# Kernel optimization log

Measured on AMD Instinct MI355X. Metric: run time of the kernel, lower is better.

## Reference

```python
import jax, jax.numpy as jnp
import numpy as np

THETA = 10000.0

def precompute_freqs_cis(dim, seq_len):
    freqs = 1.0 / THETA ** (jnp.arange(0, dim, 2)[: dim // 2].astype(jnp.float32) / dim)
    t = jnp.arange(seq_len, dtype=jnp.float32)
    ang = jnp.outer(t, freqs)  # [T, dim/2]
    return jax.lax.complex(jnp.cos(ang), jnp.sin(ang))

def apply_rope(x, freqs_cis):
    # x: [..., T, D]; freqs_cis: [T, D/2] complex
    xr = x.astype(jnp.float32).reshape(*x.shape[:-1], -1, 2)
    xc = jax.lax.complex(xr[..., 0], xr[..., 1]) * freqs_cis
    out = jnp.stack([jnp.real(xc), jnp.imag(xc)], axis=-1).reshape(x.shape)
    return out.astype(x.dtype)

def setup_inputs() -> dict:
    key = jax.random.key(0)
    k1, k2, k3, k4 = jax.random.split(key, 4)
    B, T, E, DQ, DV = 4, 2048, 1024, 128, 128
    s = 1.0 / np.sqrt(E)
    return {
        "embedding_word": jax.random.normal(k1, (B, T, E), dtype=jnp.float32),
        "w_Q": jax.random.normal(k2, (DQ, E), dtype=jnp.float32) * s,  # torch Linear weight [out,in]
        "w_K": jax.random.normal(k3, (DQ, E), dtype=jnp.float32) * s,
        "w_V": jax.random.normal(k4, (DV, E), dtype=jnp.float32) * s,
    }

def reference(embedding_word, w_Q, w_K, w_V):
    T = embedding_word.shape[-2]
    dq = w_Q.shape[0]
    q = jnp.einsum("bte,de->btd", embedding_word, w_Q)
    k = jnp.einsum("bte,de->btd", embedding_word, w_K)
    v = jnp.einsum("bte,de->btd", embedding_word, w_V)
    fc = precompute_freqs_cis(dq, T)
    q = apply_rope(q, fc)
    k = apply_rope(k, fc)
    scores = jnp.einsum("bqd,bkd->bqk", q, k)
    causal = jnp.triu(jnp.ones((T, T), dtype=bool), k=1)
    masked = jnp.where(causal, -jnp.inf, scores)
    weights = jax.nn.softmax(masked / jnp.sqrt(jnp.float32(dq)), axis=-1)
    return jnp.einsum("bqk,bkd->bqd", weights, v)
```

## Files before the change

### kernel.cpp

```cpp
#include <hip/hip_runtime.h>
#include <math.h>


#define B_ 4
#define T_ 2048
#define E_ 1024
#define D_ 128
#define BT_ (B_ * T_)

#define UNITS_PER_B 160
#define UNITS (UNITS_PER_B * B_)

typedef __bf16 bf16_t;
typedef __bf16 bf16x4 __attribute__((ext_vector_type(4)));
typedef __bf16 bf16x8 __attribute__((ext_vector_type(8)));
typedef float f32x4 __attribute__((ext_vector_type(4)));

#define GLD16(g, l)                                                         \
  __builtin_amdgcn_global_load_lds(                                         \
      (const __attribute__((address_space(1))) void*)(g),                   \
      (__attribute__((address_space(3))) void*)(l), 16, 0, 0)

__device__ __forceinline__ bf16x8 cvt8(float4 lo, float4 hi) {
  bf16x8 t;
  t[0] = (bf16_t)lo.x; t[1] = (bf16_t)lo.y; t[2] = (bf16_t)lo.z; t[3] = (bf16_t)lo.w;
  t[4] = (bf16_t)hi.x; t[5] = (bf16_t)hi.y; t[6] = (bf16_t)hi.z; t[7] = (bf16_t)hi.w;
  return t;
}
__device__ __forceinline__ bf16x8 cvt8v(f32x4 lo, f32x4 hi) {
  bf16x8 t;
  t[0] = (bf16_t)lo[0]; t[1] = (bf16_t)lo[1]; t[2] = (bf16_t)lo[2]; t[3] = (bf16_t)lo[3];
  t[4] = (bf16_t)hi[0]; t[5] = (bf16_t)hi[1]; t[6] = (bf16_t)hi[2]; t[7] = (bf16_t)hi[3];
  return t;
}

__global__ __launch_bounds__(256) void wtab_kernel(
    const float* __restrict__ Wq, const float* __restrict__ Wk,
    const float* __restrict__ Wv, bf16_t* __restrict__ Wb,
    float2* __restrict__ Tab) {
  const int gidx = blockIdx.x * 256 + threadIdx.x;
  if (gidx < 3 * D_ * E_ / 8) {
    const int z = gidx / 16384;
    const int r = gidx % 16384;
    const float* src = ((z == 0) ? Wq : (z == 1) ? Wk : Wv) + (size_t)r * 8;
    float4 u = *(const float4*)src;
    float4 v = *(const float4*)(src + 4);
    *(bf16x8*)(Wb + (size_t)z * D_ * E_ + (size_t)r * 8) = cvt8(u, v);
  }
  const float NLOG_ = -0.14391156514261485f;
  for (int idx = gidx; idx < T_ * 64; idx += 65536) {
    const int t = idx >> 6, j = idx & 63;
    const float freq = expf(NLOG_ * (float)j);
    float sn, cs;
    sincosf((float)t * freq, &sn, &cs);
    Tab[idx] = make_float2(cs, sn);
  }
}

__global__ __launch_bounds__(256) void proj64_kernel(
    const float* __restrict__ X, const bf16_t* __restrict__ Wb,
    const float2* __restrict__ Tab, bf16_t* __restrict__ Qws,
    bf16_t* __restrict__ Kws, bf16_t* __restrict__ Vtws) {
  const int o = blockIdx.x;
  const int ell = (o & 7) * 96 + (o >> 3);
  const int mt = ell / 6, ny = ell % 6;
  const int bt0 = mt * 64;

  const int tid = threadIdx.x;
  const int lane = tid & 63;
  const int wv = tid >> 6;
  const int wr = wv >> 1, wc = wv & 1;
  const int g = lane >> 4, lm = lane & 15;

  __shared__ float Axf[2][64 * 64];
  __shared__ bf16_t Bb[2][64 * 64];

  const bf16_t* Wz = Wb + (size_t)ny * 64 * E_;

  f32x4 acc[2][2];
#pragma unroll
  for (int m = 0; m < 2; m++)
#pragma unroll
    for (int n = 0; n < 2; n++) acc[m][n] = 0.0f;

  auto stage = [&](int t, int bf) {
    const int k0 = t * 64;
#pragma unroll
    for (int j = 0; j < 4; j++) {
      const int cb = (wv * 4 + j) * 64;
      const int L = cb + lane;
      const int row = L >> 4;
      const int pch = L & 15;
      const int c = pch ^ (row & 15);
      GLD16(X + (size_t)(bt0 + row) * E_ + k0 + c * 4, &Axf[bf][cb * 4]);
    }
#pragma unroll
    for (int j = 0; j < 2; j++) {
      const int cb = (wv * 2 + j) * 64;
      const int c = cb + lane;
      const int row = c >> 3;
      const int eoff = ((c & 7) * 8) ^ ((row & 7) << 3);
      GLD16(Wz + (size_t)row * E_ + k0 + eoff, &Bb[bf][cb * 8]);
    }
  };

  auto compute = [&](int bf) {
#pragma unroll
    for (int ks = 0; ks < 2; ks++) {
      const int cc = ks * 8 + g * 2;
      bf16x8 a0, a1, b0, b1;
      {
        const int r0 = wr * 32 + lm;
        f32x4 lo0 = *(const f32x4*)&Axf[bf][r0 * 64 + (cc ^ (r0 & 15)) * 4];
        f32x4 hi0 = *(const f32x4*)&Axf[bf][r0 * 64 + ((cc + 1) ^ (r0 & 15)) * 4];
        a0 = cvt8v(lo0, hi0);
        const int r1 = wr * 32 + 16 + lm;
        f32x4 lo1 = *(const f32x4*)&Axf[bf][r1 * 64 + (cc ^ (r1 & 15)) * 4];
        f32x4 hi1 = *(const f32x4*)&Axf[bf][r1 * 64 + ((cc + 1) ^ (r1 & 15)) * 4];
        a1 = cvt8v(lo1, hi1);
        const int s0 = wc * 32 + lm;
        b0 = *(const bf16x8*)&Bb[bf][s0 * 64 + ((ks * 32 + g * 8) ^ ((s0 & 7) << 3))];
        const int s1 = wc * 32 + 16 + lm;
        b1 = *(const bf16x8*)&Bb[bf][s1 * 64 + ((ks * 32 + g * 8) ^ ((s1 & 7) << 3))];
      }
      acc[0][0] = __builtin_amdgcn_mfma_f32_16x16x32_bf16(a0, b0, acc[0][0], 0, 0, 0);
      acc[0][1] = __builtin_amdgcn_mfma_f32_16x16x32_bf16(a0, b1, acc[0][1], 0, 0, 0);
      acc[1][0] = __builtin_amdgcn_mfma_f32_16x16x32_bf16(a1, b0, acc[1][0], 0, 0, 0);
      acc[1][1] = __builtin_amdgcn_mfma_f32_16x16x32_bf16(a1, b1, acc[1][1], 0, 0, 0);
    }
  };

  stage(0, 0);
  stage(1, 1);
  asm volatile("s_waitcnt vmcnt(6)" ::: "memory");
  __builtin_amdgcn_s_barrier();
  __builtin_amdgcn_sched_barrier(0);

#pragma unroll
  for (int t = 0; t < 16; t++) {
    compute(t & 1);
    __builtin_amdgcn_sched_barrier(0);
    __builtin_amdgcn_s_barrier();
    __builtin_amdgcn_sched_barrier(0);
    if (t + 2 < 16) {
      stage(t + 2, t & 1);
      asm volatile("s_waitcnt vmcnt(6)" ::: "memory");
    } else {
      asm volatile("s_waitcnt vmcnt(0)" ::: "memory");
    }
    __builtin_amdgcn_sched_barrier(0);
    __builtin_amdgcn_s_barrier();
    __builtin_amdgcn_sched_barrier(0);
  }

  const int b = bt0 >> 11;
#pragma unroll
  for (int nf = 0; nf < 2; nf++) {
    const int col = ny * 64 + wc * 32 + nf * 16 + lm;
    const int z = col >> 7;
    const int d = col & 127;
#pragma unroll
    for (int mf = 0; mf < 2; mf++) {
      const int row0 = bt0 + wr * 32 + mf * 16 + g * 4;
      if (z < 2) {
        bf16_t* dst = (z == 0) ? Qws : Kws;
#pragma unroll
        for (int r = 0; r < 4; r++) {
          const int bt = row0 + r;
          const int tt = bt & (T_ - 1);
          float val = acc[mf][nf][r];
          float prt = __shfl_xor(val, 1, 64);
          const float2 cs = Tab[(size_t)tt * 64 + (d >> 1)];
          const float outv =
              (d & 1) ? (prt * cs.y + val * cs.x) : (val * cs.x - prt * cs.y);
          dst[(size_t)bt * D_ + d] = (bf16_t)outv;
        }
      } else {
        bf16x4 pv;
#pragma unroll
        for (int r = 0; r < 4; r++) pv[r] = (bf16_t)acc[mf][nf][r];
        const int tt0 = row0 & (T_ - 1);
        *(bf16x4*)&Vtws[((size_t)(b * D_ + d)) * T_ + tt0] = pv;
      }
    }
  }
}

__global__ __launch_bounds__(128) void attn_part_kernel(
    const bf16_t* __restrict__ Qws, const bf16_t* __restrict__ Kws,
    const bf16_t* __restrict__ Vtws, float* __restrict__ Opart,
    float* __restrict__ Mpart, float* __restrict__ Lpart) {
  const int idx = blockIdx.x;
  const int b = idx / UNITS_PER_B;
  const int rem = idx % UNITS_PER_B;
  int qi, ci;
  if (rem < 16) { qi = rem; ci = 0; }
  else if (rem < 48) { int r2 = rem - 16; qi = 16 + (r2 >> 1); ci = r2 & 1; }
  else if (rem < 96) { int r2 = rem - 48; qi = 32 + r2 / 3; ci = r2 % 3; }
  else { int r2 = rem - 96; qi = 48 + (r2 >> 2); ci = r2 & 3; }
  const int slot = idx;

  const int q0 = qi * 32;
  const int tiles = (qi >> 1) + 1;
  const int t0 = ci * 8;
  const int t1 = min(t0 + 8, tiles);

  const int tid = threadIdx.x;
  const int lane = tid & 63;
  const int wv = tid >> 6;
  const int g = lane >> 4;
  const int lm = lane & 15;

  __shared__ bf16_t Ks[64 * 136];
  __shared__ bf16_t Vts[128 * 72];
  __shared__ bf16_t Ps[2 * 16 * 72];

  bf16x8 qf[4];
  {
    const bf16_t* qb = Qws + (size_t)(b * T_ + q0 + wv * 16 + lm) * D_;
#pragma unroll
    for (int kc = 0; kc < 4; kc++) qf[kc] = *(const bf16x8*)(qb + kc * 32 + g * 8);
  }

  f32x4 o[8];
#pragma unroll
  for (int i = 0; i < 8; i++) o[i] = 0.0f;
  float m_r[4], l_r[4];
#pragma unroll
  for (int r = 0; r < 4; r++) { m_r[r] = -1e30f; l_r[r] = 0.0f; }
  const float sc = 0.08838834764831845f;

  bf16x8 kreg[8], vreg[8];
  auto load_tiles = [&](int it) {
    const int k0 = it * 64;
#pragma unroll
    for (int i = 0; i < 8; i++) {
      const int c = tid + i * 128;
      kreg[i] = *(const bf16x8*)(Kws + (size_t)(b * T_ + k0 + (c >> 4)) * D_ +
                                 (c & 15) * 8);
    }
#pragma unroll
    for (int i = 0; i < 8; i++) {
      const int c = tid + i * 128;
      vreg[i] = *(const bf16x8*)(Vtws + (size_t)(b * D_ + (c >> 3)) * T_ + k0 +
                                 (c & 7) * 8);
    }
  };
  auto write_lds = [&]() {
#pragma unroll
    for (int i = 0; i < 8; i++) {
      const int c = tid + i * 128;
      *(bf16x8*)&Ks[(c >> 4) * 136 + (c & 15) * 8] = kreg[i];
    }
#pragma unroll
    for (int i = 0; i < 8; i++) {
      const int c = tid + i * 128;
      *(bf16x8*)&Vts[(c >> 3) * 72 + (c & 7) * 8] = vreg[i];
    }
  };

  load_tiles(t0);
  for (int it = t0; it < t1; it++) {
    write_lds();
    __syncthreads();
    if (it + 1 < t1) load_tiles(it + 1);

    const int k0 = it * 64;
    f32x4 s[4];
#pragma unroll
    for (int nb = 0; nb < 4; nb++) s[nb] = 0.0f;
#pragma unroll
    for (int nb = 0; nb < 4; nb++) {
#pragma unroll
      for (int kc = 0; kc < 4; kc++) {
        bf16x8 bk = *(const bf16x8*)&Ks[(nb * 16 + lm) * 136 + kc * 32 + g * 8];
        s[nb] = __builtin_amdgcn_mfma_f32_16x16x32_bf16(qf[kc], bk, s[nb], 0, 0, 0);
      }
    }

    const bool diag = (it == tiles - 1);
#pragma unroll
    for (int r = 0; r < 4; r++) {
      const int qrow = q0 + wv * 16 + g * 4 + r;
      float sv[4];
#pragma unroll
      for (int nb = 0; nb < 4; nb++) {
        sv[nb] = s[nb][r] * sc;
        if (diag && (k0 + nb * 16 + lm > qrow)) sv[nb] = -1e30f;
      }
      float tm = fmaxf(fmaxf(sv[0], sv[1]), fmaxf(sv[2], sv[3]));
      tm = fmaxf(tm, __shfl_xor(tm, 1, 64));
      tm = fmaxf(tm, __shfl_xor(tm, 2, 64));
      tm = fmaxf(tm, __shfl_xor(tm, 4, 64));
      tm = fmaxf(tm, __shfl_xor(tm, 8, 64));
      const float mnew = fmaxf(m_r[r], tm);
      const float alpha = __expf(m_r[r] - mnew);
      float p[4], rs = 0.0f;
#pragma unroll
      for (int nb = 0; nb < 4; nb++) { p[nb] = __expf(sv[nb] - mnew); rs += p[nb]; }
      rs += __shfl_xor(rs, 1, 64);
      rs += __shfl_xor(rs, 2, 64);
      rs += __shfl_xor(rs, 4, 64);
      rs += __shfl_xor(rs, 8, 64);
      l_r[r] = l_r[r] * alpha + rs;
      m_r[r] = mnew;
#pragma unroll
      for (int nb2 = 0; nb2 < 8; nb2++) o[nb2][r] *= alpha;
#pragma unroll
      for (int nb = 0; nb < 4; nb++)
        Ps[wv * 1152 + (g * 4 + r) * 72 + nb * 16 + lm] = (bf16_t)p[nb];
    }

    bf16x8 pa0 = *(const bf16x8*)&Ps[wv * 1152 + lm * 72 + g * 8];
    bf16x8 pa1 = *(const bf16x8*)&Ps[wv * 1152 + lm * 72 + 32 + g * 8];
#pragma unroll
    for (int nb2 = 0; nb2 < 8; nb2++) {
      bf16x8 bv0 = *(const bf16x8*)&Vts[(nb2 * 16 + lm) * 72 + g * 8];
      o[nb2] = __builtin_amdgcn_mfma_f32_16x16x32_bf16(pa0, bv0, o[nb2], 0, 0, 0);
      bf16x8 bv1 = *(const bf16x8*)&Vts[(nb2 * 16 + lm) * 72 + 32 + g * 8];
      o[nb2] = __builtin_amdgcn_mfma_f32_16x16x32_bf16(pa1, bv1, o[nb2], 0, 0, 0);
    }
    __syncthreads();
  }

#pragma unroll
  for (int r = 0; r < 4; r++) {
    const int row = wv * 16 + g * 4 + r;
    if (lm == 0) {
      Mpart[slot * 32 + row] = m_r[r];
      Lpart[slot * 32 + row] = l_r[r];
    }
    float* dst = Opart + ((size_t)slot * 32 + row) * D_;
#pragma unroll
    for (int nb2 = 0; nb2 < 8; nb2++) dst[nb2 * 16 + lm] = o[nb2][r];
  }
}

__global__ __launch_bounds__(256) void attn_combine_kernel(
    const float* __restrict__ Opart, const float* __restrict__ Mpart,
    const float* __restrict__ Lpart, float* __restrict__ Out) {
  const int qi = blockIdx.x;
  const int b = blockIdx.y;
  const int gg = qi >> 4;
  const int nc = gg + 1;
  const int base = b * UNITS_PER_B + ((gg * (gg + 1)) / 2) * 16 + (qi & 15) * nc;
  const int t = threadIdx.x;
  const int row = t >> 3;
  const int d0 = (t & 7) * 16;

  float mv[4];
  float mmax = -1e30f;
  for (int ci = 0; ci < nc; ci++) {
    mv[ci] = Mpart[(base + ci) * 32 + row];
    mmax = fmaxf(mmax, mv[ci]);
  }
  f32x4 acc[4];
#pragma unroll
  for (int j = 0; j < 4; j++) acc[j] = 0.0f;
  float l = 0.0f;
  for (int ci = 0; ci < nc; ci++) {
    const float w = __expf(mv[ci] - mmax);
    l += w * Lpart[(base + ci) * 32 + row];
    const float* op = Opart + ((size_t)(base + ci) * 32 + row) * D_ + d0;
#pragma unroll
    for (int j = 0; j < 4; j++) {
      float4 v = *(const float4*)(op + j * 4);
      acc[j][0] += w * v.x; acc[j][1] += w * v.y;
      acc[j][2] += w * v.z; acc[j][3] += w * v.w;
    }
  }
  const float inv = 1.0f / l;
  float* dst = Out + ((size_t)(b * T_ + qi * 32 + row)) * D_ + d0;
#pragma unroll
  for (int j = 0; j < 4; j++) {
    float4 v;
    v.x = acc[j][0] * inv; v.y = acc[j][1] * inv;
    v.z = acc[j][2] * inv; v.w = acc[j][3] * inv;
    *(float4*)(dst + j * 4) = v;
  }
}

__global__ __launch_bounds__(256) void proj_rope_kernel(
    const float* __restrict__ X, const float* __restrict__ Wq,
    const float* __restrict__ Wk, const float* __restrict__ Wv,
    bf16_t* __restrict__ Qws, bf16_t* __restrict__ Kws,
    bf16_t* __restrict__ Vtws) {
  const int z = blockIdx.y;
  const float* __restrict__ W = (z == 0) ? Wq : (z == 1) ? Wk : Wv;
  const int bt0 = blockIdx.x * 64;
  const int tid = threadIdx.x;
  const int lane = tid & 63;
  const int wv = tid >> 6;
  const int g = lane >> 4;
  const int lm = lane & 15;

  __shared__ bf16_t Xs[64 * 40];
  __shared__ bf16_t Ws[128 * 40];

  f32x4 acc[8];
#pragma unroll
  for (int i = 0; i < 8; i++) acc[i] = 0.0f;

  for (int kk = 0; kk < E_ / 32; kk++) {
    {
      const int row = tid >> 2, c0 = (tid & 3) * 8;
      const float* src = X + (size_t)(bt0 + row) * E_ + kk * 32 + c0;
      float4 u = *(const float4*)src;
      float4 v = *(const float4*)(src + 4);
      *(bf16x8*)&Xs[row * 40 + c0] = cvt8(u, v);
    }
#pragma unroll
    for (int h = 0; h < 2; h++) {
      const int cc = tid * 2 + h;
      const int row = cc >> 2, c0 = (cc & 3) * 8;
      const float* src = W + (size_t)row * E_ + kk * 32 + c0;
      float4 u = *(const float4*)src;
      float4 v = *(const float4*)(src + 4);
      *(bf16x8*)&Ws[row * 40 + c0] = cvt8(u, v);
    }
    __syncthreads();
    bf16x8 a = *(const bf16x8*)&Xs[(wv * 16 + lm) * 40 + g * 8];
#pragma unroll
    for (int nb = 0; nb < 8; nb++) {
      bf16x8 bb = *(const bf16x8*)&Ws[(nb * 16 + lm) * 40 + g * 8];
      acc[nb] = __builtin_amdgcn_mfma_f32_16x16x32_bf16(a, bb, acc[nb], 0, 0, 0);
    }
    __syncthreads();
  }
  const float NLOG_ = -0.14391156514261485f;
#pragma unroll
  for (int nb = 0; nb < 8; nb++) {
    const int col = nb * 16 + lm;
    const float freq = expf(NLOG_ * (float)(col >> 1));
#pragma unroll
    for (int r = 0; r < 4; r++) {
      const int bt = bt0 + wv * 16 + g * 4 + r;
      float val = acc[nb][r];
      float prt = __shfl_xor(val, 1, 64);
      if (z < 2) {
        const int t = bt & (T_ - 1);
        const float ang = (float)t * freq;
        float sn, cs;
        sincosf(ang, &sn, &cs);
        const float outv = (col & 1) ? (prt * sn + val * cs) : (val * cs - prt * sn);
        bf16_t* dst = (z == 0) ? Qws : Kws;
        dst[(size_t)bt * D_ + col] = (bf16_t)outv;
      } else {
        const int b = bt >> 11, t = bt & (T_ - 1);
        Vtws[((size_t)(b * D_ + col)) * T_ + t] = (bf16_t)val;
      }
    }
  }
}

__global__ __launch_bounds__(128) void attn_kernel(
    const bf16_t* __restrict__ Qws, const bf16_t* __restrict__ Kws,
    const bf16_t* __restrict__ Vtws, float* __restrict__ Out) {
  const int b = blockIdx.y;
  const int qi = blockIdx.x;
  const int q0 = qi * 32;
  const int tid = threadIdx.x;
  const int lane = tid & 63;
  const int wv = tid >> 6;
  const int g = lane >> 4;
  const int lm = lane & 15;

  __shared__ bf16_t Ks[32 * 136];
  __shared__ bf16_t Vts[128 * 40];
  __shared__ bf16_t Ps[2 * 16 * 40];

  bf16x8 qf[4];
  {
    const bf16_t* qb = Qws + (size_t)(b * T_ + q0 + wv * 16 + lm) * D_;
#pragma unroll
    for (int kk = 0; kk < 4; kk++) qf[kk] = *(const bf16x8*)(qb + kk * 32 + g * 8);
  }
  f32x4 o[8];
#pragma unroll
  for (int i = 0; i < 8; i++) o[i] = 0.0f;
  float m_r[4], l_r[4];
#pragma unroll
  for (int r = 0; r < 4; r++) { m_r[r] = -1e30f; l_r[r] = 0.0f; }
  const float sc = 0.08838834764831845f;

  for (int kt = 0; kt <= qi; kt++) {
    const int kv0 = kt * 32;
#pragma unroll
    for (int i = 0; i < 4; i++) {
      const int c = tid + i * 128;
      const int row = c >> 4, part = c & 15;
      bf16x8 v = *(const bf16x8*)(Kws + (size_t)(b * T_ + kv0 + row) * D_ + part * 8);
      *(bf16x8*)&Ks[row * 136 + part * 8] = v;
    }
#pragma unroll
    for (int i = 0; i < 4; i++) {
      const int c = tid + i * 128;
      const int d = c >> 2, part = c & 3;
      bf16x8 v = *(const bf16x8*)(Vtws + (size_t)(b * D_ + d) * T_ + kv0 + part * 8);
      *(bf16x8*)&Vts[d * 40 + part * 8] = v;
    }
    __syncthreads();
    f32x4 s[2];
    s[0] = 0.0f; s[1] = 0.0f;
#pragma unroll
    for (int nb = 0; nb < 2; nb++) {
#pragma unroll
      for (int kc = 0; kc < 4; kc++) {
        bf16x8 bk = *(const bf16x8*)&Ks[(nb * 16 + lm) * 136 + kc * 32 + g * 8];
        s[nb] = __builtin_amdgcn_mfma_f32_16x16x32_bf16(qf[kc], bk, s[nb], 0, 0, 0);
      }
    }
    const bool diag = (kt == qi);
#pragma unroll
    for (int r = 0; r < 4; r++) {
      float sv0 = s[0][r] * sc;
      float sv1 = s[1][r] * sc;
      if (diag) {
        const int rowr = wv * 16 + g * 4 + r;
        if (lm > rowr) sv0 = -1e30f;
        if (lm + 16 > rowr) sv1 = -1e30f;
      }
      float tm = fmaxf(sv0, sv1);
      tm = fmaxf(tm, __shfl_xor(tm, 1, 64));
      tm = fmaxf(tm, __shfl_xor(tm, 2, 64));
      tm = fmaxf(tm, __shfl_xor(tm, 4, 64));
      tm = fmaxf(tm, __shfl_xor(tm, 8, 64));
      const float mnew = fmaxf(m_r[r], tm);
      const float alpha = __expf(m_r[r] - mnew);
      const float p0 = __expf(sv0 - mnew);
      const float p1 = __expf(sv1 - mnew);
      float rs = p0 + p1;
      rs += __shfl_xor(rs, 1, 64);
      rs += __shfl_xor(rs, 2, 64);
      rs += __shfl_xor(rs, 4, 64);
      rs += __shfl_xor(rs, 8, 64);
      l_r[r] = l_r[r] * alpha + rs;
      m_r[r] = mnew;
#pragma unroll
      for (int nb2 = 0; nb2 < 8; nb2++) o[nb2][r] *= alpha;
      Ps[wv * 640 + (g * 4 + r) * 40 + lm] = (bf16_t)p0;
      Ps[wv * 640 + (g * 4 + r) * 40 + 16 + lm] = (bf16_t)p1;
    }
    bf16x8 pa = *(const bf16x8*)&Ps[wv * 640 + lm * 40 + g * 8];
#pragma unroll
    for (int nb2 = 0; nb2 < 8; nb2++) {
      bf16x8 bv = *(const bf16x8*)&Vts[(nb2 * 16 + lm) * 40 + g * 8];
      o[nb2] = __builtin_amdgcn_mfma_f32_16x16x32_bf16(pa, bv, o[nb2], 0, 0, 0);
    }
    __syncthreads();
  }
#pragma unroll
  for (int r = 0; r < 4; r++) {
    const float inv = 1.0f / l_r[r];
    float* dst = Out + (size_t)(b * T_ + q0 + wv * 16 + g * 4 + r) * D_;
#pragma unroll
    for (int nb2 = 0; nb2 < 8; nb2++) dst[nb2 * 16 + lm] = o[nb2][r] * inv;
  }
}

extern "C" void kernel_launch(void* const* d_in, const int* in_sizes, int n_in,
                              void* d_out, int out_size, void* d_ws,
                              size_t ws_size, hipStream_t stream) {
  const float* X = (const float*)d_in[0];
  const float* Wq = (const float*)d_in[1];
  const float* Wk = (const float*)d_in[2];
  const float* Wv = (const float*)d_in[3];
  float* Out = (float*)d_out;

  const size_t wb_bytes = (size_t)3 * D_ * E_ * sizeof(bf16_t);
  const size_t qkv_bytes = (size_t)3 * BT_ * D_ * sizeof(bf16_t);
  const size_t opart_bytes = (size_t)UNITS * 32 * D_ * sizeof(float);
  const size_t ml_bytes = (size_t)UNITS * 32 * sizeof(float);
  const size_t tab_bytes = (size_t)T_ * 64 * sizeof(float2);

  const size_t needA =
      wb_bytes + qkv_bytes + opart_bytes + 2 * ml_bytes + tab_bytes;
  const size_t needB = qkv_bytes + opart_bytes + 2 * ml_bytes;

  if (ws_size >= needA) {
    bf16_t* Wb = (bf16_t*)d_ws;
    bf16_t* Qws = Wb + (size_t)3 * D_ * E_;
    bf16_t* Kws = Qws + (size_t)BT_ * D_;
    bf16_t* Vtws = Kws + (size_t)BT_ * D_;
    float* Opart = (float*)((char*)d_ws + wb_bytes + qkv_bytes);
    float* Mpart = (float*)((char*)Opart + opart_bytes);
    float* Lpart = (float*)((char*)Mpart + ml_bytes);
    float2* Tab = (float2*)((char*)Lpart + ml_bytes);

    hipLaunchKernelGGL(wtab_kernel, dim3(256), dim3(256), 0, stream,
                       Wq, Wk, Wv, Wb, Tab);
    hipLaunchKernelGGL(proj64_kernel, dim3(768), dim3(256), 0, stream,
                       X, Wb, Tab, Qws, Kws, Vtws);
    hipLaunchKernelGGL(attn_part_kernel, dim3(UNITS), dim3(128), 0, stream,
                       Qws, Kws, Vtws, Opart, Mpart, Lpart);
    hipLaunchKernelGGL(attn_combine_kernel, dim3(T_ / 32, B_), dim3(256), 0,
                       stream, Opart, Mpart, Lpart, Out);
  } else if (ws_size >= needB) {
    bf16_t* Qws = (bf16_t*)d_ws;
    bf16_t* Kws = Qws + (size_t)BT_ * D_;
    bf16_t* Vtws = Kws + (size_t)BT_ * D_;
    float* Opart = (float*)((char*)d_ws + qkv_bytes);
    float* Mpart = (float*)((char*)Opart + opart_bytes);
    float* Lpart = (float*)((char*)Mpart + ml_bytes);
    hipLaunchKernelGGL(proj_rope_kernel, dim3(BT_ / 64, 3), dim3(256), 0,
                       stream, X, Wq, Wk, Wv, Qws, Kws, Vtws);
    hipLaunchKernelGGL(attn_part_kernel, dim3(UNITS), dim3(128), 0, stream,
                       Qws, Kws, Vtws, Opart, Mpart, Lpart);
    hipLaunchKernelGGL(attn_combine_kernel, dim3(T_ / 32, B_), dim3(256), 0,
                       stream, Opart, Mpart, Lpart, Out);
  } else {
    bf16_t* Qws = (bf16_t*)d_ws;
    bf16_t* Kws = Qws + (size_t)BT_ * D_;
    bf16_t* Vtws = Kws + (size_t)BT_ * D_;
    hipLaunchKernelGGL(proj_rope_kernel, dim3(BT_ / 64, 3), dim3(256), 0,
                       stream, X, Wq, Wk, Wv, Qws, Kws, Vtws);
    hipLaunchKernelGGL(attn_kernel, dim3(T_ / 32, B_), dim3(128), 0, stream,
                       Qws, Kws, Vtws, Out);
  }
}
```

Before: 58.38 us.

## Enlarge projection tile to 128x96 with 512 threads and split loader waves

Replaces the 64x64-tile projection GEMM (768 blocks of 256 threads) with a 128x96 tile (256 blocks of 512 threads). Half the waves load X tiles and half load W tiles, each with its own vmcnt wait. The larger tile cuts redundant global reads of X and W and gives each wave a 2x3 MFMA fragment. In exchange, LDS use per block roughly doubles and only 256 blocks run, so there is only one block per CU and fewer waves to hide latency.

```diff
diff --git a/kernel.cpp b/kernel.cpp
--- a/kernel.cpp
+++ b/kernel.cpp
@@ -57,82 +57,93 @@
   }
 }
 
-__global__ __launch_bounds__(256) void proj64_kernel(
+__global__ __launch_bounds__(512, 1) void proj128_kernel(
     const float* __restrict__ X, const bf16_t* __restrict__ Wb,
     const float2* __restrict__ Tab, bf16_t* __restrict__ Qws,
     bf16_t* __restrict__ Kws, bf16_t* __restrict__ Vtws) {
   const int o = blockIdx.x;
-  const int ell = (o & 7) * 96 + (o >> 3);
-  const int mt = ell / 6, ny = ell % 6;
-  const int bt0 = mt * 64;
+  const int ell = (o & 7) * 32 + (o >> 3);
+  const int mt = ell >> 2, ny = ell & 3;
+  const int bt0 = mt * 128;
 
   const int tid = threadIdx.x;
   const int lane = tid & 63;
   const int wv = tid >> 6;
-  const int wr = wv >> 1, wc = wv & 1;
+  const int wr = wv >> 1, wcn = wv & 1;
   const int g = lane >> 4, lm = lane & 15;
 
-  __shared__ float Axf[2][64 * 64];
-  __shared__ bf16_t Bb[2][64 * 64];
-
-  const bf16_t* Wz = Wb + (size_t)ny * 64 * E_;
-
-  f32x4 acc[2][2];
+  __shared__ float Axf[2][128 * 64];
+  __shared__ bf16_t Bb[2][96 * 64];
+
+  const bf16_t* Wz = Wb + (size_t)ny * 96 * E_;
+
+  f32x4 acc[2][3];
 #pragma unroll
   for (int m = 0; m < 2; m++)
 #pragma unroll
-    for (int n = 0; n < 2; n++) acc[m][n] = 0.0f;
+    for (int n = 0; n < 3; n++) acc[m][n] = 0.0f;
 
   auto stage = [&](int t, int bf) {
     const int k0 = t * 64;
-#pragma unroll
-    for (int j = 0; j < 4; j++) {
-      const int cb = (wv * 4 + j) * 64;
-      const int L = cb + lane;
-      const int row = L >> 4;
-      const int pch = L & 15;
-      const int c = pch ^ (row & 15);
-      GLD16(X + (size_t)(bt0 + row) * E_ + k0 + c * 4, &Axf[bf][cb * 4]);
-    }
-#pragma unroll
-    for (int j = 0; j < 2; j++) {
-      const int cb = (wv * 2 + j) * 64;
-      const int c = cb + lane;
-      const int row = c >> 3;
-      const int eoff = ((c & 7) * 8) ^ ((row & 7) << 3);
-      GLD16(Wz + (size_t)row * E_ + k0 + eoff, &Bb[bf][cb * 8]);
+    if (wv < 4) {
+#pragma unroll
+      for (int j = 0; j < 8; j++) {
+        const int cb = (wv * 8 + j) * 64;
+        const int L = cb + lane;
+        const int row = L >> 4;
+        const int pch = L & 15;
+        const int c = pch ^ (row & 15);
+        GLD16(X + (size_t)(bt0 + row) * E_ + k0 + c * 4, &Axf[bf][cb * 4]);
+      }
+    } else {
+#pragma unroll
+      for (int j = 0; j < 3; j++) {
+        const int cb = ((wv - 4) * 3 + j) * 64;
+        const int c = cb + lane;
+        const int row = c >> 3;
+        const int eoff = ((c & 7) * 8) ^ ((row & 7) << 3);
+        GLD16(Wz + (size_t)row * E_ + k0 + eoff, &Bb[bf][cb * 8]);
+      }
     }
   };
+
+#define WAITSTAGE()                                                          \
+  do {                                                                       \
+    if (wv < 4)                                                              \
+      asm volatile("s_waitcnt vmcnt(8)" ::: "memory");                       \
+    else                                                                     \
+      asm volatile("s_waitcnt vmcnt(3)" ::: "memory");                       \
+  } while (0)
 
   auto compute = [&](int bf) {
 #pragma unroll
     for (int ks = 0; ks < 2; ks++) {
       const int cc = ks * 8 + g * 2;
-      bf16x8 a0, a1, b0, b1;
-      {
-        const int r0 = wr * 32 + lm;
-        f32x4 lo0 = *(const f32x4*)&Axf[bf][r0 * 64 + (cc ^ (r0 & 15)) * 4];
-        f32x4 hi0 = *(const f32x4*)&Axf[bf][r0 * 64 + ((cc + 1) ^ (r0 & 15)) * 4];
-        a0 = cvt8v(lo0, hi0);
-        const int r1 = wr * 32 + 16 + lm;
-        f32x4 lo1 = *(const f32x4*)&Axf[bf][r1 * 64 + (cc ^ (r1 & 15)) * 4];
-        f32x4 hi1 = *(const f32x4*)&Axf[bf][r1 * 64 + ((cc + 1) ^ (r1 & 15)) * 4];
-        a1 = cvt8v(lo1, hi1);
-        const int s0 = wc * 32 + lm;
-        b0 = *(const bf16x8*)&Bb[bf][s0 * 64 + ((ks * 32 + g * 8) ^ ((s0 & 7) << 3))];
-        const int s1 = wc * 32 + 16 + lm;
-        b1 = *(const bf16x8*)&Bb[bf][s1 * 64 + ((ks * 32 + g * 8) ^ ((s1 & 7) << 3))];
-      }
-      acc[0][0] = __builtin_amdgcn_mfma_f32_16x16x32_bf16(a0, b0, acc[0][0], 0, 0, 0);
-      acc[0][1] = __builtin_amdgcn_mfma_f32_16x16x32_bf16(a0, b1, acc[0][1], 0, 0, 0);
-      acc[1][0] = __builtin_amdgcn_mfma_f32_16x16x32_bf16(a1, b0, acc[1][0], 0, 0, 0);
-      acc[1][1] = __builtin_amdgcn_mfma_f32_16x16x32_bf16(a1, b1, acc[1][1], 0, 0, 0);
+      bf16x8 a[2], b[3];
+#pragma unroll
+      for (int mf = 0; mf < 2; mf++) {
+        const int r = wr * 32 + mf * 16 + lm;
+        f32x4 lo = *(const f32x4*)&Axf[bf][r * 64 + ((cc) ^ (r & 15)) * 4];
+        f32x4 hi = *(const f32x4*)&Axf[bf][r * 64 + ((cc + 1) ^ (r & 15)) * 4];
+        a[mf] = cvt8v(lo, hi);
+      }
+#pragma unroll
+      for (int nf = 0; nf < 3; nf++) {
+        const int s = wcn * 48 + nf * 16 + lm;
+        b[nf] = *(const bf16x8*)&Bb[bf][s * 64 + ((ks * 32 + g * 8) ^ ((s & 7) << 3))];
+      }
+#pragma unroll
+      for (int mf = 0; mf < 2; mf++)
+#pragma unroll
+        for (int nf = 0; nf < 3; nf++)
+          acc[mf][nf] = __builtin_amdgcn_mfma_f32_16x16x32_bf16(
+              a[mf], b[nf], acc[mf][nf], 0, 0, 0);
     }
   };
 
   stage(0, 0);
   stage(1, 1);
-  asm volatile("s_waitcnt vmcnt(6)" ::: "memory");
+  WAITSTAGE();
   __builtin_amdgcn_s_barrier();
   __builtin_amdgcn_sched_barrier(0);
 
@@ -144,7 +155,7 @@
     __builtin_amdgcn_sched_barrier(0);
     if (t + 2 < 16) {
       stage(t + 2, t & 1);
-      asm volatile("s_waitcnt vmcnt(6)" ::: "memory");
+      WAITSTAGE();
     } else {
       asm volatile("s_waitcnt vmcnt(0)" ::: "memory");
     }
@@ -155,8 +166,8 @@
 
   const int b = bt0 >> 11;
 #pragma unroll
-  for (int nf = 0; nf < 2; nf++) {
-    const int col = ny * 64 + wc * 32 + nf * 16 + lm;
+  for (int nf = 0; nf < 3; nf++) {
+    const int col = ny * 96 + wcn * 48 + nf * 16 + lm;
     const int z = col >> 7;
     const int d = col & 127;
 #pragma unroll
@@ -184,6 +195,7 @@
       }
     }
   }
+#undef WAITSTAGE
 }
 
 __global__ __launch_bounds__(128) void attn_part_kernel(
@@ -589,7 +601,7 @@
 
     hipLaunchKernelGGL(wtab_kernel, dim3(256), dim3(256), 0, stream,
                        Wq, Wk, Wv, Wb, Tab);
-    hipLaunchKernelGGL(proj64_kernel, dim3(768), dim3(256), 0, stream,
+    hipLaunchKernelGGL(proj128_kernel, dim3(256), dim3(512), 0, stream,
                        X, Wb, Tab, Qws, Kws, Vtws);
     hipLaunchKernelGGL(attn_part_kernel, dim3(UNITS), dim3(128), 0, stream,
                        Qws, Kws, Vtws, Opart, Mpart, Lpart);
```

After: 61.56 us. +5.5%, slower.

## Enlarge attention query tile to 64 rows per block for K/V reuse

Applied to the files above, without the earlier changes.

The split-KV attention kernel now processes 64 query rows per block (32 per wave, two MFMA row fragments) instead of 32, so each K/V tile loaded into LDS serves twice as many queries. The work decomposition changes from 160 to 80 units per batch, and the combine kernel is rewritten for the new partition layout with 512 threads. This halves K/V global traffic and LDS staging per query, at the cost of fewer blocks in flight, higher register pressure, and coarser causal load balancing. The intermediate workspace fallback path is also dropped.

```diff
diff --git a/kernel.cpp b/kernel.cpp
--- a/kernel.cpp
+++ b/kernel.cpp
@@ -8,8 +8,8 @@
 #define D_ 128
 #define BT_ (B_ * T_)
 
-#define UNITS_PER_B 160
-#define UNITS (UNITS_PER_B * B_)
+#define UNITS2_PER_B 80
+#define UNITS2 (UNITS2_PER_B * B_)
 
 typedef __bf16 bf16_t;
 typedef __bf16 bf16x4 __attribute__((ext_vector_type(4)));
@@ -186,22 +186,24 @@
   }
 }
 
-__global__ __launch_bounds__(128) void attn_part_kernel(
+__global__ __launch_bounds__(128) void attn_part2_kernel(
     const bf16_t* __restrict__ Qws, const bf16_t* __restrict__ Kws,
     const bf16_t* __restrict__ Vtws, float* __restrict__ Opart,
     float* __restrict__ Mpart, float* __restrict__ Lpart) {
   const int idx = blockIdx.x;
-  const int b = idx / UNITS_PER_B;
-  const int rem = idx % UNITS_PER_B;
-  int qi, ci;
-  if (rem < 16) { qi = rem; ci = 0; }
-  else if (rem < 48) { int r2 = rem - 16; qi = 16 + (r2 >> 1); ci = r2 & 1; }
-  else if (rem < 96) { int r2 = rem - 48; qi = 32 + r2 / 3; ci = r2 % 3; }
-  else { int r2 = rem - 96; qi = 48 + (r2 >> 2); ci = r2 & 3; }
+  const int b = idx / UNITS2_PER_B;
+  int rem = idx % UNITS2_PER_B;
+  int qi2 = 0, ci = 0;
+#pragma unroll 1
+  for (int q = 0; q < 32; q++) {
+    const int nc = (q + 8) >> 3;
+    if (rem < nc) { qi2 = q; ci = rem; break; }
+    rem -= nc;
+  }
   const int slot = idx;
 
-  const int q0 = qi * 32;
-  const int tiles = (qi >> 1) + 1;
+  const int q0 = qi2 * 64;
+  const int tiles = qi2 + 1;
   const int t0 = ci * 8;
   const int t1 = min(t0 + 8, tiles);
 
@@ -213,21 +215,28 @@
 
   __shared__ bf16_t Ks[64 * 136];
   __shared__ bf16_t Vts[128 * 72];
-  __shared__ bf16_t Ps[2 * 16 * 72];
-
-  bf16x8 qf[4];
-  {
-    const bf16_t* qb = Qws + (size_t)(b * T_ + q0 + wv * 16 + lm) * D_;
-#pragma unroll
-    for (int kc = 0; kc < 4; kc++) qf[kc] = *(const bf16x8*)(qb + kc * 32 + g * 8);
-  }
-
-  f32x4 o[8];
-#pragma unroll
-  for (int i = 0; i < 8; i++) o[i] = 0.0f;
-  float m_r[4], l_r[4];
-#pragma unroll
-  for (int r = 0; r < 4; r++) { m_r[r] = -1e30f; l_r[r] = 0.0f; }
+  __shared__ bf16_t Ps[2 * 32 * 72];
+
+  bf16x8 qf[2][4];
+#pragma unroll
+  for (int mf = 0; mf < 2; mf++) {
+    const bf16_t* qb =
+        Qws + (size_t)(b * T_ + q0 + wv * 32 + mf * 16 + lm) * D_;
+#pragma unroll
+    for (int kc = 0; kc < 4; kc++)
+      qf[mf][kc] = *(const bf16x8*)(qb + kc * 32 + g * 8);
+  }
+
+  f32x4 o[2][8];
+#pragma unroll
+  for (int mf = 0; mf < 2; mf++)
+#pragma unroll
+    for (int i = 0; i < 8; i++) o[mf][i] = 0.0f;
+  float m_r[2][4], l_r[2][4];
+#pragma unroll
+  for (int mf = 0; mf < 2; mf++)
+#pragma unroll
+    for (int r = 0; r < 4; r++) { m_r[mf][r] = -1e30f; l_r[mf][r] = 0.0f; }
   const float sc = 0.08838834764831845f;
 
   bf16x8 kreg[8], vreg[8];
@@ -266,84 +275,101 @@
     if (it + 1 < t1) load_tiles(it + 1);
 
     const int k0 = it * 64;
-    f32x4 s[4];
-#pragma unroll
-    for (int nb = 0; nb < 4; nb++) s[nb] = 0.0f;
+    f32x4 s[2][4];
+#pragma unroll
+    for (int mf = 0; mf < 2; mf++)
+#pragma unroll
+      for (int nb = 0; nb < 4; nb++) s[mf][nb] = 0.0f;
 #pragma unroll
     for (int nb = 0; nb < 4; nb++) {
 #pragma unroll
       for (int kc = 0; kc < 4; kc++) {
         bf16x8 bk = *(const bf16x8*)&Ks[(nb * 16 + lm) * 136 + kc * 32 + g * 8];
-        s[nb] = __builtin_amdgcn_mfma_f32_16x16x32_bf16(qf[kc], bk, s[nb], 0, 0, 0);
+        s[0][nb] = __builtin_amdgcn_mfma_f32_16x16x32_bf16(qf[0][kc], bk, s[0][nb], 0, 0, 0);
+        s[1][nb] = __builtin_amdgcn_mfma_f32_16x16x32_bf16(qf[1][kc], bk, s[1][nb], 0, 0, 0);
       }
     }
 
     const bool diag = (it == tiles - 1);
 #pragma unroll
-    for (int r = 0; r < 4; r++) {
-      const int qrow = q0 + wv * 16 + g * 4 + r;
-      float sv[4];
-#pragma unroll
-      for (int nb = 0; nb < 4; nb++) {
-        sv[nb] = s[nb][r] * sc;
-        if (diag && (k0 + nb * 16 + lm > qrow)) sv[nb] = -1e30f;
-      }
-      float tm = fmaxf(fmaxf(sv[0], sv[1]), fmaxf(sv[2], sv[3]));
-      tm = fmaxf(tm, __shfl_xor(tm, 1, 64));
-      tm = fmaxf(tm, __shfl_xor(tm, 2, 64));
-      tm = fmaxf(tm, __shfl_xor(tm, 4, 64));
-      tm = fmaxf(tm, __shfl_xor(tm, 8, 64));
-      const float mnew = fmaxf(m_r[r], tm);
-      const float alpha = __expf(m_r[r] - mnew);
-      float p[4], rs = 0.0f;
-#pragma unroll
-      for (int nb = 0; nb < 4; nb++) { p[nb] = __expf(sv[nb] - mnew); rs += p[nb]; }
-      rs += __shfl_xor(rs, 1, 64);
-      rs += __shfl_xor(rs, 2, 64);
-      rs += __shfl_xor(rs, 4, 64);
-      rs += __shfl_xor(rs, 8, 64);
-      l_r[r] = l_r[r] * alpha + rs;
-      m_r[r] = mnew;
-#pragma unroll
-      for (int nb2 = 0; nb2 < 8; nb2++) o[nb2][r] *= alpha;
-#pragma unroll
-      for (int nb = 0; nb < 4; nb++)
-        Ps[wv * 1152 + (g * 4 + r) * 72 + nb * 16 + lm] = (bf16_t)p[nb];
-    }
-
-    bf16x8 pa0 = *(const bf16x8*)&Ps[wv * 1152 + lm * 72 + g * 8];
-    bf16x8 pa1 = *(const bf16x8*)&Ps[wv * 1152 + lm * 72 + 32 + g * 8];
+    for (int mf = 0; mf < 2; mf++) {
+#pragma unroll
+      for (int r = 0; r < 4; r++) {
+        const int qrow = q0 + wv * 32 + mf * 16 + g * 4 + r;
+        float sv[4];
+#pragma unroll
+        for (int nb = 0; nb < 4; nb++) {
+          sv[nb] = s[mf][nb][r] * sc;
+          if (diag && (k0 + nb * 16 + lm > qrow)) sv[nb] = -1e30f;
+        }
+        float tm = fmaxf(fmaxf(sv[0], sv[1]), fmaxf(sv[2], sv[3]));
+        tm = fmaxf(tm, __shfl_xor(tm, 1, 64));
+        tm = fmaxf(tm, __shfl_xor(tm, 2, 64));
+        tm = fmaxf(tm, __shfl_xor(tm, 4, 64));
+        tm = fmaxf(tm, __shfl_xor(tm, 8, 64));
+        const float mnew = fmaxf(m_r[mf][r], tm);
+        const float alpha = __expf(m_r[mf][r] - mnew);
+        float p[4], rs = 0.0f;
+#pragma unroll
+        for (int nb = 0; nb < 4; nb++) { p[nb] = __expf(sv[nb] - mnew); rs += p[nb]; }
+        rs += __shfl_xor(rs, 1, 64);
+        rs += __shfl_xor(rs, 2, 64);
+        rs += __shfl_xor(rs, 4, 64);
+        rs += __shfl_xor(rs, 8, 64);
+        l_r[mf][r] = l_r[mf][r] * alpha + rs;
+        m_r[mf][r] = mnew;
+#pragma unroll
+        for (int nb2 = 0; nb2 < 8; nb2++) o[mf][nb2][r] *= alpha;
+#pragma unroll
+        for (int nb = 0; nb < 4; nb++)
+          Ps[wv * 2304 + (mf * 16 + g * 4 + r) * 72 + nb * 16 + lm] = (bf16_t)p[nb];
+      }
+    }
+
+    bf16x8 pa[2][2];
+#pragma unroll
+    for (int mf = 0; mf < 2; mf++) {
+      pa[mf][0] = *(const bf16x8*)&Ps[wv * 2304 + (mf * 16 + lm) * 72 + g * 8];
+      pa[mf][1] = *(const bf16x8*)&Ps[wv * 2304 + (mf * 16 + lm) * 72 + 32 + g * 8];
+    }
 #pragma unroll
     for (int nb2 = 0; nb2 < 8; nb2++) {
       bf16x8 bv0 = *(const bf16x8*)&Vts[(nb2 * 16 + lm) * 72 + g * 8];
-      o[nb2] = __builtin_amdgcn_mfma_f32_16x16x32_bf16(pa0, bv0, o[nb2], 0, 0, 0);
       bf16x8 bv1 = *(const bf16x8*)&Vts[(nb2 * 16 + lm) * 72 + 32 + g * 8];
-      o[nb2] = __builtin_amdgcn_mfma_f32_16x16x32_bf16(pa1, bv1, o[nb2], 0, 0, 0);
+#pragma unroll
+      for (int mf = 0; mf < 2; mf++) {
+        o[mf][nb2] = __builtin_amdgcn_mfma_f32_16x16x32_bf16(pa[mf][0], bv0, o[mf][nb2], 0, 0, 0);
+        o[mf][nb2] = __builtin_amdgcn_mfma_f32_16x16x32_bf16(pa[mf][1], bv1, o[mf][nb2], 0, 0, 0);
+      }
     }
     __syncthreads();
   }
 
 #pragma unroll
-  for (int r = 0; r < 4; r++) {
-    const int row = wv * 16 + g * 4 + r;
-    if (lm == 0) {
-      Mpart[slot * 32 + row] = m_r[r];
-      Lpart[slot * 32 + row] = l_r[r];
-    }
-    float* dst = Opart + ((size_t)slot * 32 + row) * D_;
-#pragma unroll
-    for (int nb2 = 0; nb2 < 8; nb2++) dst[nb2 * 16 + lm] = o[nb2][r];
-  }
-}
-
-__global__ __launch_bounds__(256) void attn_combine_kernel(
+  for (int mf = 0; mf < 2; mf++) {
+#pragma unroll
+    for (int r = 0; r < 4; r++) {
+      const int row = wv * 32 + mf * 16 + g * 4 + r;
+      if (lm == 0) {
+        Mpart[slot * 64 + row] = m_r[mf][r];
+        Lpart[slot * 64 + row] = l_r[mf][r];
+      }
+      float* dst = Opart + ((size_t)slot * 64 + row) * D_;
+#pragma unroll
+      for (int nb2 = 0; nb2 < 8; nb2++) dst[nb2 * 16 + lm] = o[mf][nb2][r];
+    }
+  }
+}
+
+__global__ __launch_bounds__(512) void attn_combine2_kernel(
     const float* __restrict__ Opart, const float* __restrict__ Mpart,
     const float* __restrict__ Lpart, float* __restrict__ Out) {
-  const int qi = blockIdx.x;
+  const int qi2 = blockIdx.x;
   const int b = blockIdx.y;
-  const int gg = qi >> 4;
-  const int nc = gg + 1;
-  const int base = b * UNITS_PER_B + ((gg * (gg + 1)) / 2) * 16 + (qi & 15) * nc;
+  const int nc = (qi2 + 8) >> 3;
+  const int a = qi2 >> 3, rr = qi2 & 7;
+  const int cum = 4 * a * (a + 1) + rr * (a + 1);
+  const int base = b * UNITS2_PER_B + cum;
   const int t = threadIdx.x;
   const int row = t >> 3;
   const int d0 = (t & 7) * 16;
@@ -351,7 +377,7 @@
   float mv[4];
   float mmax = -1e30f;
   for (int ci = 0; ci < nc; ci++) {
-    mv[ci] = Mpart[(base + ci) * 32 + row];
+    mv[ci] = Mpart[(base + ci) * 64 + row];
     mmax = fmaxf(mmax, mv[ci]);
   }
   f32x4 acc[4];
@@ -360,8 +386,8 @@
   float l = 0.0f;
   for (int ci = 0; ci < nc; ci++) {
     const float w = __expf(mv[ci] - mmax);
-    l += w * Lpart[(base + ci) * 32 + row];
-    const float* op = Opart + ((size_t)(base + ci) * 32 + row) * D_ + d0;
+    l += w * Lpart[(base + ci) * 64 + row];
+    const float* op = Opart + ((size_t)(base + ci) * 64 + row) * D_ + d0;
 #pragma unroll
     for (int j = 0; j < 4; j++) {
       float4 v = *(const float4*)(op + j * 4);
@@ -370,7 +396,7 @@
     }
   }
   const float inv = 1.0f / l;
-  float* dst = Out + ((size_t)(b * T_ + qi * 32 + row)) * D_ + d0;
+  float* dst = Out + ((size_t)(b * T_ + qi2 * 64 + row)) * D_ + d0;
 #pragma unroll
   for (int j = 0; j < 4; j++) {
     float4 v;
@@ -569,13 +595,13 @@
 
   const size_t wb_bytes = (size_t)3 * D_ * E_ * sizeof(bf16_t);
   const size_t qkv_bytes = (size_t)3 * BT_ * D_ * sizeof(bf16_t);
-  const size_t opart_bytes = (size_t)UNITS * 32 * D_ * sizeof(float);
-  const size_t ml_bytes = (size_t)UNITS * 32 * sizeof(float);
+  const size_t opart_bytes = (size_t)UNITS2 * 64 * D_ * sizeof(float);
+  const size_t ml_bytes = (size_t)UNITS2 * 64 * sizeof(float);
   const size_t tab_bytes = (size_t)T_ * 64 * sizeof(float2);
 
   const size_t needA =
       wb_bytes + qkv_bytes + opart_bytes + 2 * ml_bytes + tab_bytes;
-  const size_t needB = qkv_bytes + opart_bytes + 2 * ml_bytes;
+  const size_t needB = qkv_bytes;
 
   if (ws_size >= needA) {
     bf16_t* Wb = (bf16_t*)d_ws;
@@ -591,24 +617,11 @@
                        Wq, Wk, Wv, Wb, Tab);
     hipLaunchKernelGGL(proj64_kernel, dim3(768), dim3(256), 0, stream,
                        X, Wb, Tab, Qws, Kws, Vtws);
-    hipLaunchKernelGGL(attn_part_kernel, dim3(UNITS), dim3(128), 0, stream,
+    hipLaunchKernelGGL(attn_part2_kernel, dim3(UNITS2), dim3(128), 0, stream,
                        Qws, Kws, Vtws, Opart, Mpart, Lpart);
-    hipLaunchKernelGGL(attn_combine_kernel, dim3(T_ / 32, B_), dim3(256), 0,
+    hipLaunchKernelGGL(attn_combine2_kernel, dim3(32, B_), dim3(512), 0,
                        stream, Opart, Mpart, Lpart, Out);
   } else if (ws_size >= needB) {
-    bf16_t* Qws = (bf16_t*)d_ws;
-    bf16_t* Kws = Qws + (size_t)BT_ * D_;
-    bf16_t* Vtws = Kws + (size_t)BT_ * D_;
-    float* Opart = (float*)((char*)d_ws + qkv_bytes);
-    float* Mpart = (float*)((char*)Opart + opart_bytes);
-    float* Lpart = (float*)((char*)Mpart + ml_bytes);
-    hipLaunchKernelGGL(proj_rope_kernel, dim3(BT_ / 64, 3), dim3(256), 0,
-                       stream, X, Wq, Wk, Wv, Qws, Kws, Vtws);
-    hipLaunchKernelGGL(attn_part_kernel, dim3(UNITS), dim3(128), 0, stream,
-                       Qws, Kws, Vtws, Opart, Mpart, Lpart);
-    hipLaunchKernelGGL(attn_combine_kernel, dim3(T_ / 32, B_), dim3(256), 0,
-                       stream, Opart, Mpart, Lpart, Out);
-  } else {
     bf16_t* Qws = (bf16_t*)d_ws;
     bf16_t* Kws = Qws + (size_t)BT_ * D_;
     bf16_t* Vtws = Kws + (size_t)BT_ * D_;
```

After: 69.21 us. 1.19x slower.
